# Performance work log

Hardware: AMD Instinct MI355X
Metric: run time of the kernel (lower is better)

## Reference

```python
import jax, jax.numpy as jnp
import numpy as np

EPS = 1e-8
B, S1, S2, D, H, L, NCLS = 4, 256, 256, 300, 256, 10, 22
AGG_IN = 2 + 3 * 2 * L  # cos max/mean + (maxpool, attentive, max-attentive) x (fw,bw) x l = 62


def _lstm_dir(x, Wih, Whh, b):
    # x: (batch, seq, in); PyTorch gate order i, f, g, o
    pre = jnp.einsum('bsd,gd->bsg', x, Wih) + b
    h0 = jnp.zeros((x.shape[0], Whh.shape[1]), x.dtype)
    def step(carry, p):
        h, c = carry
        g = p + h @ Whh.T
        i, f, gg, o = jnp.split(g, 4, axis=-1)
        c = jax.nn.sigmoid(f) * c + jax.nn.sigmoid(i) * jnp.tanh(gg)
        h = jax.nn.sigmoid(o) * jnp.tanh(c)
        return (h, c), h
    (hT, _), hs = jax.lax.scan(step, (h0, h0), jnp.swapaxes(pre, 0, 1))
    return jnp.swapaxes(hs, 0, 1), hT


def bilstm(x, Wf, Uf, bf, Wb, Ub, bb):
    hs_f, hT_f = _lstm_dir(x, Wf, Uf, bf)
    hs_b, hT_b = _lstm_dir(x[:, ::-1], Wb, Ub, bb)
    return jnp.concatenate([hs_f, hs_b[:, ::-1]], -1), hT_f, hT_b


def div_small(n, d):
    return n / jnp.where(d > EPS, d, EPS)


def cos_matrix(v1, v2):
    # (b,p,h),(b,q,h) -> (b,p,q) cosine similarity matrix (attention())
    a = jnp.einsum('bph,bqh->bpq', v1, v2)
    d = jnp.linalg.norm(v1, axis=-1)[:, :, None] * jnp.linalg.norm(v2, axis=-1)[:, None, :]
    return div_small(a, d)


def mp_match(v1, v2, w):
    # mp_matching_func: cosine over h of (w*v1, w*v2) per perspective -> (b,s,l)
    w2 = w * w
    num = jnp.einsum('lh,bsh,bsh->bsl', w2, v1, v2)
    n1 = jnp.sqrt(jnp.einsum('lh,bsh->bsl', w2, v1 * v1))
    n2 = jnp.sqrt(jnp.einsum('lh,bsh->bsl', w2, v2 * v2))
    return num / jnp.maximum(n1 * n2, EPS)


def mp_match_pairwise(v1, v2, w):
    # mp_matching_func_pairwise -> (b,p,q,l)
    v1w = v1[:, None] * w[None, :, None]  # (b,l,p,h)
    v2w = v2[:, None] * w[None, :, None]  # (b,l,q,h)
    n = jnp.einsum('blph,blqh->blpq', v1w, v2w)
    d = jnp.linalg.norm(v1w, axis=-1)[:, :, :, None] * jnp.linalg.norm(v2w, axis=-1)[:, :, None, :]
    return jnp.transpose(div_small(n, d), (0, 2, 3, 1))


def bimpm_forward(left, right,
                  ctx_Wih_f, ctx_Whh_f, ctx_b_f, ctx_Wih_b, ctx_Whh_b, ctx_b_b,
                  agg_Wih_f, agg_Whh_f, agg_b_f, agg_Wih_b, agg_Whh_b, agg_b_b,
                  mp_w3, mp_w4, mp_w5, mp_w6, mp_w7, mp_w8,
                  fc1_W, fc1_b, fc2_W, fc2_b):
    cp, _, _ = bilstm(left, ctx_Wih_f, ctx_Whh_f, ctx_b_f, ctx_Wih_b, ctx_Whh_b, ctx_b_b)
    ch, _, _ = bilstm(right, ctx_Wih_f, ctx_Whh_f, ctx_b_f, ctx_Wih_b, ctx_Whh_b, ctx_b_b)
    p_fw, p_bw = jnp.split(cp, 2, -1)  # (b,p,H) each
    h_fw, h_bw = jnp.split(ch, 2, -1)  # (b,q,H) each
    att_fw = cos_matrix(p_fw, h_fw)  # also the cosine_sim used for max/mean match
    att_bw = cos_matrix(p_bw, h_bw)
    mv1 = [att_fw.max(2, keepdims=True), att_fw.mean(2, keepdims=True)]
    mv2 = [att_fw.max(1)[..., None], att_fw.mean(1)[..., None]]
    # maxpool match
    mm_fw = mp_match_pairwise(p_fw, h_fw, mp_w3)
    mm_bw = mp_match_pairwise(p_bw, h_bw, mp_w4)
    mv1 += [mm_fw.max(2), mm_bw.max(2)]
    mv2 += [mm_fw.max(1), mm_bw.max(1)]
    # attentive + max-attentive match
    def att_stats(att, vp, vh):
        mean_h = div_small(jnp.einsum('bpq,bqh->bph', att, vh), att.sum(2, keepdims=True))
        mean_p = div_small(jnp.einsum('bpq,bph->bqh', att, vp), att.sum(1)[..., None])
        max_h = jnp.max(att[..., None] * vh[:, None, :, :], axis=2)  # (b,p,H)
        max_p = jnp.max(att[..., None] * vp[:, :, None, :], axis=1)  # (b,q,H)
        return mean_h, mean_p, max_h, max_p
    mh_fw, mpv_fw, xh_fw, xp_fw = att_stats(att_fw, p_fw, h_fw)
    mh_bw, mpv_bw, xh_bw, xp_bw = att_stats(att_bw, p_bw, h_bw)
    mv1 += [mp_match(p_fw, mh_fw, mp_w5), mp_match(p_bw, mh_bw, mp_w6),
            mp_match(p_fw, xh_fw, mp_w7), mp_match(p_bw, xh_bw, mp_w8)]
    mv2 += [mp_match(h_fw, mpv_fw, mp_w5), mp_match(h_bw, mpv_bw, mp_w6),
            mp_match(h_fw, xp_fw, mp_w7), mp_match(h_bw, xp_bw, mp_w8)]
    mv_p = jnp.concatenate(mv1, -1)  # (b,p,62)
    mv_h = jnp.concatenate(mv2, -1)  # (b,q,62)
    _, ap_f, ap_b = bilstm(mv_p, agg_Wih_f, agg_Whh_f, agg_b_f, agg_Wih_b, agg_Whh_b, agg_b_b)
    _, ah_f, ah_b = bilstm(mv_h, agg_Wih_f, agg_Whh_f, agg_b_f, agg_Wih_b, agg_Whh_b, agg_b_b)
    l1, l2 = left.shape[1], right.shape[1]
    lengths = jnp.broadcast_to(jnp.array([l1 / (l1 + l2), l2 / (l1 + l2)], left.dtype), (left.shape[0], 2))
    x = jnp.concatenate([ap_f, ap_b, ah_f, ah_b, lengths, left.mean(1), right.mean(1)], -1)
    x = jnp.tanh(x @ fc1_W.T + fc1_b)
    return x @ fc2_W.T + fc2_b


def setup_inputs():
    ks = jax.random.split(jax.random.key(0), 20)
    f = lambda i, shape, s=0.1: jax.random.normal(ks[i], shape, jnp.float32) * s
    return {
        'left': jax.random.normal(ks[0], (B, S1, D), jnp.float32),
        'right': jax.random.normal(ks[1], (B, S2, D), jnp.float32),
        'ctx_Wih_f': f(2, (4 * H, D)), 'ctx_Whh_f': f(3, (4 * H, H)), 'ctx_b_f': jnp.zeros((4 * H,), jnp.float32),
        'ctx_Wih_b': f(4, (4 * H, D)), 'ctx_Whh_b': f(5, (4 * H, H)), 'ctx_b_b': jnp.zeros((4 * H,), jnp.float32),
        'agg_Wih_f': f(6, (4 * H, AGG_IN)), 'agg_Whh_f': f(7, (4 * H, H)), 'agg_b_f': jnp.zeros((4 * H,), jnp.float32),
        'agg_Wih_b': f(8, (4 * H, AGG_IN)), 'agg_Whh_b': f(9, (4 * H, H)), 'agg_b_b': jnp.zeros((4 * H,), jnp.float32),
        'mp_w3': f(10, (L, H), 0.3), 'mp_w4': f(11, (L, H), 0.3), 'mp_w5': f(12, (L, H), 0.3),
        'mp_w6': f(13, (L, H), 0.3), 'mp_w7': f(14, (L, H), 0.3), 'mp_w8': f(15, (L, H), 0.3),
        'fc1_W': f(16, (2 * H, 4 * H + 2 + 2 * D), 0.01), 'fc1_b': jnp.zeros((2 * H,), jnp.float32),
        'fc2_W': f(17, (NCLS, 2 * H), 0.01), 'fc2_b': jnp.zeros((NCLS,), jnp.float32),
    }


def reference(left, right, ctx_Wih_f, ctx_Whh_f, ctx_b_f, ctx_Wih_b, ctx_Whh_b, ctx_b_b,
              agg_Wih_f, agg_Whh_f, agg_b_f, agg_Wih_b, agg_Whh_b, agg_b_b,
              mp_w3, mp_w4, mp_w5, mp_w6, mp_w7, mp_w8, fc1_W, fc1_b, fc2_W, fc2_b):
    return bimpm_forward(left, right, ctx_Wih_f, ctx_Whh_f, ctx_b_f, ctx_Wih_b, ctx_Whh_b, ctx_b_b,
                         agg_Wih_f, agg_Whh_f, agg_b_f, agg_Wih_b, agg_Whh_b, agg_b_b,
                         mp_w3, mp_w4, mp_w5, mp_w6, mp_w7, mp_w8, fc1_W, fc1_b, fc2_W, fc2_b)
```

## Files before the change

kernel.cpp:

```cpp
#include <hip/hip_runtime.h>
#include <hip/hip_bf16.h>
#include <math.h>

#define EPSV 1e-8f

__device__ __forceinline__ float dsmall(float d){ return d > EPSV ? d : EPSV; }
__device__ __forceinline__ float sigf(float x){ return 1.f/(1.f+expf(-x)); }

__global__ __launch_bounds__(1024) void k_transpose2(const float* __restrict__ WF,
                                                     const float* __restrict__ WB,
                                                     float* __restrict__ WT0,
                                                     float* __restrict__ WT1){
  const float* W = blockIdx.z ? WB : WF;
  float* WT = blockIdx.z ? WT1 : WT0;
  __shared__ float t[32][33];
  int rb = blockIdx.y*32, cb = blockIdx.x*32;
  int r = rb + threadIdx.y, c = cb + threadIdx.x;
  t[threadIdx.y][threadIdx.x] = W[(size_t)r*256 + c];
  __syncthreads();
  int rr = cb + threadIdx.y, cc = rb + threadIdx.x;
  WT[(size_t)rr*1024 + cc] = t[threadIdx.x][threadIdx.y];
}

__global__ __launch_bounds__(256) void k_proj(
    const float* __restrict__ left, const float* __restrict__ right,
    const float* __restrict__ WihF, const float* __restrict__ WihB,
    const float* __restrict__ bF, const float* __restrict__ bB,
    float* __restrict__ PREf, float* __restrict__ PREb)
{
  const int z = blockIdx.z, zo = z >> 1, zi = z & 1;
  const float* A = zo ? right : left;
  const float* B = zi ? WihB : WihF;
  const float* bias = zi ? bB : bF;
  float* C = (zi ? PREb : PREf) + (size_t)zo*1048576;
  const int K = 300;

  __shared__ float As[16][68];
  __shared__ float Bs[16][68];
  const int mb = blockIdx.y*64, nb = blockIdx.x*64;
  const int tid = threadIdx.x;
  const int tx = tid & 15, ty = tid >> 4;

  float acc[4][4];
  #pragma unroll
  for (int i=0;i<4;i++)
    #pragma unroll
    for (int j=0;j<4;j++) acc[i][j] = 0.f;

  for (int kt = 0; kt < K; kt += 16) {
    int ka = tid & 15, ma = tid >> 4;
    #pragma unroll
    for (int q=0;q<4;q++){
      int m = ma + q*16;
      float v = 0.f, bvv = 0.f;
      if (kt+ka < K){
        v = A[(size_t)(mb+m)*300 + kt+ka];
        bvv = B[(size_t)(nb+m)*300 + kt+ka];
      }
      As[ka][m] = v; Bs[ka][m] = bvv;
    }
    __syncthreads();
    #pragma unroll
    for (int k=0;k<16;k++){
      float a[4], bv[4];
      #pragma unroll
      for (int i=0;i<4;i++) a[i] = As[k][ty*4+i];
      #pragma unroll
      for (int j=0;j<4;j++) bv[j] = Bs[k][tx*4+j];
      #pragma unroll
      for (int i=0;i<4;i++)
        #pragma unroll
        for (int j=0;j<4;j++) acc[i][j] += a[i]*bv[j];
    }
    __syncthreads();
  }
  #pragma unroll
  for (int i=0;i<4;i++){
    int m = mb + ty*4 + i;
    #pragma unroll
    for (int j=0;j<4;j++){
      int n = nb + tx*4 + j;
      C[(size_t)m*1024 + n] = acc[i][j] + bias[n];
    }
  }
}

__global__ __launch_bounds__(256) void k_aggproj(
    const float* __restrict__ MV_,
    const float* __restrict__ WihF, const float* __restrict__ WihB,
    const float* __restrict__ bF, const float* __restrict__ bB,
    float* __restrict__ PREf, float* __restrict__ PREb)
{
  const int zi = blockIdx.z;
  const float* B = zi ? WihB : WihF;
  const float* bias = zi ? bB : bF;
  float* C = zi ? PREb : PREf;
  const int K = 62;

  __shared__ float As[16][68];
  __shared__ float Bs[16][68];
  const int mb = blockIdx.y*64, nb = blockIdx.x*64;
  const int tid = threadIdx.x;
  const int tx = tid & 15, ty = tid >> 4;

  float acc[4][4];
  #pragma unroll
  for (int i=0;i<4;i++)
    #pragma unroll
    for (int j=0;j<4;j++) acc[i][j] = 0.f;

  for (int kt = 0; kt < K; kt += 16) {
    int ka = tid & 15, ma = tid >> 4;
    #pragma unroll
    for (int q=0;q<4;q++){
      int m = ma + q*16;
      float v = 0.f, bvv = 0.f;
      if (kt+ka < K){
        v = MV_[(size_t)(mb+m)*62 + kt+ka];
        bvv = B[(size_t)(nb+m)*62 + kt+ka];
      }
      As[ka][m] = v; Bs[ka][m] = bvv;
    }
    __syncthreads();
    #pragma unroll
    for (int k=0;k<16;k++){
      float a[4], bv[4];
      #pragma unroll
      for (int i=0;i<4;i++) a[i] = As[k][ty*4+i];
      #pragma unroll
      for (int j=0;j<4;j++) bv[j] = Bs[k][tx*4+j];
      #pragma unroll
      for (int i=0;i<4;i++)
        #pragma unroll
        for (int j=0;j<4;j++) acc[i][j] += a[i]*bv[j];
    }
    __syncthreads();
  }
  #pragma unroll
  for (int i=0;i<4;i++){
    int m = mb + ty*4 + i;
    #pragma unroll
    for (int j=0;j<4;j++){
      int n = nb + tx*4 + j;
      C[(size_t)m*1024 + n] = acc[i][j] + bias[n];
    }
  }
}

__global__ __launch_bounds__(256) void k_att(
    const float* __restrict__ HS_, const float* __restrict__ NORM_,
    float* __restrict__ ATT_)
{
  const int z = blockIdx.z;
  const int d = z >> 2, b = z & 3;
  const float* A = HS_ + d*256 + (size_t)b*131072;
  const float* B = HS_ + 524288 + d*256 + (size_t)b*131072;
  const float* Uv = NORM_ + (size_t)b*512 + d*256;
  const float* Vv = NORM_ + (size_t)(4+b)*512 + d*256;
  float* C = ATT_ + (size_t)z*65536;

  __shared__ float As[16][68];
  __shared__ float Bs[16][68];
  const int mb = blockIdx.y*64, nb = blockIdx.x*64;
  const int tid = threadIdx.x;
  const int tx = tid & 15, ty = tid >> 4;

  float acc[4][4];
  #pragma unroll
  for (int i=0;i<4;i++)
    #pragma unroll
    for (int j=0;j<4;j++) acc[i][j] = 0.f;

  for (int kt = 0; kt < 256; kt += 16) {
    int ka = tid & 15, ma = tid >> 4;
    #pragma unroll
    for (int q=0;q<4;q++){
      int m = ma + q*16;
      As[ka][m] = A[(size_t)(mb+m)*512 + kt+ka];
      Bs[ka][m] = B[(size_t)(nb+m)*512 + kt+ka];
    }
    __syncthreads();
    #pragma unroll
    for (int k=0;k<16;k++){
      float a[4], bv[4];
      #pragma unroll
      for (int i=0;i<4;i++) a[i] = As[k][ty*4+i];
      #pragma unroll
      for (int j=0;j<4;j++) bv[j] = Bs[k][tx*4+j];
      #pragma unroll
      for (int i=0;i<4;i++)
        #pragma unroll
        for (int j=0;j<4;j++) acc[i][j] += a[i]*bv[j];
    }
    __syncthreads();
  }
  #pragma unroll
  for (int i=0;i<4;i++){
    int m = mb + ty*4 + i;
    float um = Uv[m];
    #pragma unroll
    for (int j=0;j<4;j++){
      int n = nb + tx*4 + j;
      C[(size_t)m*256 + n] = acc[i][j] / dsmall(um * Vv[n]);
    }
  }
}

__global__ __launch_bounds__(256) void k_attstat(
    const float* __restrict__ ATT_, const float* __restrict__ HS_,
    const float* __restrict__ RS_, const float* __restrict__ CS_,
    float* __restrict__ MEANH_, float* __restrict__ XH_,
    float* __restrict__ MEANP_, float* __restrict__ XP_)
{
  const int z16 = blockIdx.z;
  const int var = z16 >> 3;
  const int z = z16 & 7;
  const int d = z >> 2, b = z & 3;
  const float* A = ATT_ + (size_t)z*65536;
  const float* B = (var ? HS_ : HS_ + 524288) + d*256 + (size_t)b*131072;
  const float* U = (var ? CS_ : RS_) + z*256;
  float* C1 = (var ? MEANP_ : MEANH_) + (size_t)z*65536;
  float* C2 = (var ? XP_    : XH_   ) + (size_t)z*65536;

  __shared__ float As[16][68];
  __shared__ float Bs[16][68];
  const int mb = blockIdx.y*64, nb = blockIdx.x*64;
  const int tid = threadIdx.x;
  const int tx = tid & 15, ty = tid >> 4;

  float asum[4][4], amax[4][4];
  #pragma unroll
  for (int i=0;i<4;i++)
    #pragma unroll
    for (int j=0;j<4;j++){ asum[i][j]=0.f; amax[i][j]=-INFINITY; }

  for (int kt = 0; kt < 256; kt += 16) {
    if (var == 0) {
      int ka = tid & 15, ma = tid >> 4;
      #pragma unroll
      for (int q=0;q<4;q++)
        As[ka][ma+q*16] = A[(size_t)(mb+ma+q*16)*256 + kt+ka];
    } else {
      int ma = tid & 63, ka = tid >> 6;
      #pragma unroll
      for (int q=0;q<4;q++)
        As[ka+q*4][ma] = A[(size_t)(kt+ka+q*4)*256 + mb+ma];
    }
    {
      int nbi = tid & 63, kb = tid >> 6;
      #pragma unroll
      for (int q=0;q<4;q++)
        Bs[kb+q*4][nbi] = B[(size_t)(kt+kb+q*4)*512 + nb+nbi];
    }
    __syncthreads();
    #pragma unroll
    for (int k=0;k<16;k++){
      float a[4], bv[4];
      #pragma unroll
      for (int i=0;i<4;i++) a[i] = As[k][ty*4+i];
      #pragma unroll
      for (int j=0;j<4;j++) bv[j] = Bs[k][tx*4+j];
      #pragma unroll
      for (int i=0;i<4;i++)
        #pragma unroll
        for (int j=0;j<4;j++){
          float p = a[i]*bv[j];
          asum[i][j] += p;
          amax[i][j] = fmaxf(amax[i][j], p);
        }
    }
    __syncthreads();
  }
  #pragma unroll
  for (int i=0;i<4;i++){
    int m = mb + ty*4 + i;
    float ud = dsmall(U[m]);
    #pragma unroll
    for (int j=0;j<4;j++){
      int n = nb + tx*4 + j;
      C1[(size_t)m*256 + n] = asum[i][j] / ud;
      C2[(size_t)m*256 + n] = amax[i][j];
    }
  }
}

__global__ __launch_bounds__(256) void k_pmm2(
    const float* __restrict__ HS_,
    const float* __restrict__ w3, const float* __restrict__ w4,
    const float* __restrict__ WN1_, const float* __restrict__ WN2_,
    float* __restrict__ PARTR, float* __restrict__ PARTC)
{
  const int z = blockIdx.z;
  const int dir = z >= 40;
  const int zz = z - dir*40;
  const int bq = zz / 10, l = zz % 10;
  const float* A = HS_ + dir*256 + (size_t)bq*131072;
  const float* B = HS_ + 524288 + dir*256 + (size_t)bq*131072;
  const float* Wv = (dir ? w4 : w3) + l*256;
  const float* U = WN1_ + dir*10240 + bq*2560 + l*256;
  const float* V = WN2_ + dir*10240 + bq*2560 + l*256;

  __shared__ float As[16][68];
  __shared__ float Bs[16][68];
  const int mb = blockIdx.y*64, nb = blockIdx.x*64;
  const int tid = threadIdx.x;
  const int tx = tid & 15, ty = tid >> 4;

  float acc[4][4];
  #pragma unroll
  for (int i=0;i<4;i++)
    #pragma unroll
    for (int j=0;j<4;j++) acc[i][j] = 0.f;

  for (int kt = 0; kt < 256; kt += 16) {
    int ka = tid & 15, ma = tid >> 4;
    float w = Wv[kt+ka]; float w2 = w*w;
    #pragma unroll
    for (int q=0;q<4;q++){
      As[ka][ma+q*16] = A[(size_t)(mb+ma+q*16)*512 + kt+ka] * w2;
      Bs[ka][ma+q*16] = B[(size_t)(nb+ma+q*16)*512 + kt+ka];
    }
    __syncthreads();
    #pragma unroll
    for (int k=0;k<16;k++){
      float a[4], bv[4];
      #pragma unroll
      for (int i=0;i<4;i++) a[i] = As[k][ty*4+i];
      #pragma unroll
      for (int j=0;j<4;j++) bv[j] = Bs[k][tx*4+j];
      #pragma unroll
      for (int i=0;i<4;i++)
        #pragma unroll
        for (int j=0;j<4;j++) acc[i][j] += a[i]*bv[j];
    }
    __syncthreads();
  }
  float um[4], vn[4];
  #pragma unroll
  for (int i=0;i<4;i++) um[i] = U[mb + ty*4 + i];
  #pragma unroll
  for (int j=0;j<4;j++) vn[j] = V[nb + tx*4 + j];
  float c[4][4];
  #pragma unroll
  for (int i=0;i<4;i++)
    #pragma unroll
    for (int j=0;j<4;j++) c[i][j] = acc[i][j] / dsmall(um[i]*vn[j]);

  float rm[4];
  #pragma unroll
  for (int i=0;i<4;i++){
    rm[i] = fmaxf(fmaxf(c[i][0], c[i][1]), fmaxf(c[i][2], c[i][3]));
    rm[i] = fmaxf(rm[i], __shfl_xor(rm[i], 1, 64));
    rm[i] = fmaxf(rm[i], __shfl_xor(rm[i], 2, 64));
    rm[i] = fmaxf(rm[i], __shfl_xor(rm[i], 4, 64));
    rm[i] = fmaxf(rm[i], __shfl_xor(rm[i], 8, 64));
  }
  if ((tid & 15) == 0){
    #pragma unroll
    for (int i=0;i<4;i++)
      PARTR[((size_t)z*4 + blockIdx.x)*256 + mb + ty*4 + i] = rm[i];
  }
  __syncthreads();
  float* colp = &As[0][0];
  #pragma unroll
  for (int j=0;j<4;j++)
    colp[ty*64 + tx*4 + j] = fmaxf(fmaxf(c[0][j], c[1][j]), fmaxf(c[2][j], c[3][j]));
  __syncthreads();
  if (tid < 64){
    float m = colp[tid];
    #pragma unroll
    for (int r=1;r<16;r++) m = fmaxf(m, colp[r*64 + tid]);
    PARTC[((size_t)z*4 + blockIdx.y)*256 + nb + tid] = m;
  }
}

__global__ void k_pcomb(const float* __restrict__ PARTR, const float* __restrict__ PARTC,
                        float* __restrict__ MMRo, float* __restrict__ MMCo){
  int z = blockIdx.x, i = threadIdx.x;
  size_t b0 = (size_t)z*4*256 + i;
  float r = fmaxf(fmaxf(PARTR[b0], PARTR[b0+256]), fmaxf(PARTR[b0+512], PARTR[b0+768]));
  float c = fmaxf(fmaxf(PARTC[b0], PARTC[b0+256]), fmaxf(PARTC[b0+512], PARTC[b0+768]));
  MMRo[(size_t)z*256 + i] = r;
  MMCo[(size_t)z*256 + i] = c;
}

__global__ __launch_bounds__(256, 1) void k_scanaux(
    const float* __restrict__ PREf, const float* __restrict__ PREb,
    const float* __restrict__ WTf, const float* __restrict__ WTb,
    float* __restrict__ Hbuf, int* __restrict__ flg,
    float* __restrict__ HSo, float* __restrict__ HTo,
    int do_aux,
    const float* __restrict__ fc1W, float* __restrict__ W1T,
    const float* __restrict__ aWhhF, float* __restrict__ WTaggF,
    const float* __restrict__ aWhhB, float* __restrict__ WTaggB,
    const float* __restrict__ left, const float* __restrict__ right,
    float* __restrict__ XM)
{
  __shared__ float Wl[256][128];
  __shared__ float hl[256];
  __shared__ float red[4][4][40];

  const int bx = blockIdx.x;
  const int tid = threadIdx.x;

  if (bx >= 128) {
    if (!do_aux) return;
    float (*tl)[33] = (float(*)[33])Wl;
    const int aux = bx - 128;
    for (int u = aux; u < 816 + 512 + 8; u += 64) {
      if (u < 816) {
        int tI = u % 16, tJ = u / 16;
        int r0 = tI*32, c0 = tJ*32;
        for (int e = tid; e < 1024; e += 256) {
          int rr = e >> 5, cc = e & 31;
          int c = c0 + cc;
          tl[rr][cc] = (c < 1626) ? fc1W[(size_t)(r0+rr)*1626 + c] : 0.f;
        }
        __syncthreads();
        for (int e = tid; e < 1024; e += 256) {
          int cc = e >> 5, rr = e & 31;
          int c = c0 + cc;
          if (c < 1626) W1T[(size_t)c*512 + r0 + rr] = tl[rr][cc];
        }
        __syncthreads();
      } else if (u < 1328) {
        int u2 = u - 816;
        const float* S = (u2 >= 256) ? aWhhB : aWhhF;
        float* D = (u2 >= 256) ? WTaggB : WTaggF;
        int tile = u2 & 255;
        int r0 = (tile >> 3)*32, c0 = (tile & 7)*32;
        for (int e = tid; e < 1024; e += 256) {
          int rr = e >> 5, cc = e & 31;
          tl[rr][cc] = S[(size_t)(r0+rr)*256 + c0 + cc];
        }
        __syncthreads();
        for (int e = tid; e < 1024; e += 256) {
          int cc = e >> 5, rr = e & 31;
          D[(size_t)(c0+cc)*1024 + r0 + rr] = tl[rr][cc];
        }
        __syncthreads();
      } else {
        int m = u - 1328;
        int b = m & 3, sideR = m >> 2;
        const float* src = sideR ? right : left;
        for (int ch = tid; ch < 300; ch += 256) {
          float s = 0.f;
          for (int t = 0; t < 256; t++) s += src[((size_t)(b*256+t))*300 + ch];
          XM[b*600 + sideR*300 + ch] = s * (1.f/256.f);
        }
      }
    }
    return;
  }

  const int team = bx & 15;
  const int d  = team >> 3;
  const int sq = team & 7;
  const int wg = bx >> 4;
  const float* PRE = d ? PREb : PREf;
  const float* WT  = d ? WTb  : WTf;
  float* Hb = Hbuf + (size_t)team*512;
  int* fl = flg + team*256;

  const int kc = tid >> 5;
  const int gq = tid & 31;
  const int aj = tid & 31;

  for (int e = tid; e < 256*128; e += 256) {
    int k = e >> 7, c = e & 127;
    Wl[k][c] = WT[(size_t)k*1024 + (c>>5)*256 + wg*32 + (c&31)];
  }
  if (tid < 256) hl[tid] = 0.f;
  float cst = 0.f;
  __syncthreads();

  for (int tt = 0; tt < 256; ++tt) {
    const int t = d ? 255 - tt : tt;
    const int wp = tt & 1;
    const int sp = (tt + 1) & 1;

    float pre0=0.f, pre1=0.f, pre2=0.f, pre3=0.f;
    if (tid < 32) {
      const size_t pbase = ((size_t)(sq*256 + t))*1024 + wg*32 + aj;
      pre0 = PRE[pbase];       pre1 = PRE[pbase + 256];
      pre2 = PRE[pbase + 512]; pre3 = PRE[pbase + 768];
    }

    if (tt > 0 && kc != wg) {
      const int* flp = &fl[kc*32];
      while (__hip_atomic_load(flp, __ATOMIC_RELAXED, __HIP_MEMORY_SCOPE_AGENT) < tt)
        __builtin_amdgcn_s_sleep(1);
      float v = __hip_atomic_load(&Hb[sp*256 + kc*32 + gq],
                                  __ATOMIC_RELAXED, __HIP_MEMORY_SCOPE_AGENT);
      hl[kc*32 + gq] = v;
    }

    float acc[4] = {0.f, 0.f, 0.f, 0.f};
    #pragma unroll 8
    for (int kk = 0; kk < 32; ++kk) {
      const int k = kc*32 + kk;
      float4 w = *(const float4*)&Wl[k][gq*4];
      float h = hl[k];
      acc[0] += h*w.x; acc[1] += h*w.y; acc[2] += h*w.z; acc[3] += h*w.w;
    }
    #pragma unroll
    for (int c2=0;c2<4;c2++)
      acc[c2] += __shfl_xor(acc[c2], 32, 64);
    if ((tid & 32) == 0) {
      const int kp = kc >> 1;
      #pragma unroll
      for (int c2=0;c2<4;c2++)
        red[kp][c2][gq] = acc[c2];
    }
    __syncthreads();

    float hreg = 0.f;
    if (tid < 32) {
      float g[4];
      #pragma unroll
      for (int gt=0; gt<4; ++gt) {
        const int c = gt*32 + aj;
        const int gqq = c >> 2, cc = c & 3;
        g[gt] = red[0][cc][gqq] + red[1][cc][gqq] + red[2][cc][gqq] + red[3][cc][gqq];
      }
      g[0] += pre0; g[1] += pre1; g[2] += pre2; g[3] += pre3;
      const float ig = sigf(g[0]), fg = sigf(g[1]), gg = tanhf(g[2]), og = sigf(g[3]);
      cst = fg*cst + ig*gg;
      hreg = og*tanhf(cst);
      hl[wg*32 + aj] = hreg;
      __hip_atomic_store(&Hb[wp*256 + wg*32 + aj], hreg,
                         __ATOMIC_RELAXED, __HIP_MEMORY_SCOPE_AGENT);
    }
    __syncthreads();

    if (tid == 0)
      __hip_atomic_store(&fl[wg*32], tt+1, __ATOMIC_RELAXED, __HIP_MEMORY_SCOPE_AGENT);

    if (tid < 32) {
      if (HSo) HSo[((size_t)(sq*256 + t))*512 + d*256 + wg*32 + aj] = hreg;
      if (HTo && tt == 255) HTo[((size_t)(sq*2 + d))*256 + wg*32 + aj] = hreg;
    }
  }
}

__global__ __launch_bounds__(256) void k_norms(const float* __restrict__ HS_,
                                               const float* __restrict__ w3, const float* __restrict__ w4,
                                               float* __restrict__ NORM_,
                                               float* __restrict__ WN1_, float* __restrict__ WN2_){
  const int bx = blockIdx.x;
  int lane = threadIdx.x & 63;
  if (bx < 1024) {
    int r = bx*4 + (threadIdx.x >> 6);
    int seq = r >> 9, d = (r >> 8) & 1, i = r & 255;
    const float* row = HS_ + ((size_t)(seq*256 + i))*512 + d*256;
    float s = 0.f;
    #pragma unroll
    for (int q=0;q<4;q++){ float v = row[lane + 64*q]; s += v*v; }
    for (int off=32; off; off>>=1) s += __shfl_xor(s, off, 64);
    if (lane == 0) NORM_[r] = sqrtf(s);
  } else {
    int rid = (bx-1024)*4 + (threadIdx.x >> 6);
    int side = rid / 20480; int rem = rid % 20480;
    int d = rem / 10240; int rem2 = rem % 10240;
    int b = rem2 / 2560; int l = (rem2 / 256) % 10; int i = rem2 & 255;
    int seq = side ? 4+b : b;
    const float* row = HS_ + ((size_t)(seq*256 + i))*512 + d*256;
    const float* w = (d ? w4 : w3) + l*256;
    float s = 0.f;
    #pragma unroll
    for (int q=0;q<4;q++){ float wv = w[lane+64*q]; float v = row[lane+64*q]; s += wv*wv*v*v; }
    for (int off=32; off; off>>=1) s += __shfl_xor(s, off, 64);
    if (lane == 0) (side ? WN2_ : WN1_)[rem] = sqrtf(s);
  }
}

__global__ __launch_bounds__(256) void k_redcomb(const float* __restrict__ ATT_,
                                                 float* __restrict__ RS_, float* __restrict__ RMAX_,
                                                 float* __restrict__ CS_, float* __restrict__ CMAX_){
  const int bx = blockIdx.x;
  if (bx < 512) {
    int r = bx*4 + (threadIdx.x >> 6);
    int lane = threadIdx.x & 63;
    const float* row = ATT_ + (size_t)r*256;
    float s = 0.f, m = -INFINITY;
    #pragma unroll
    for (int q=0;q<4;q++){ float v = row[lane + 64*q]; s += v; m = fmaxf(m,v); }
    for (int off=32; off; off>>=1){ s += __shfl_xor(s,off,64); m = fmaxf(m, __shfl_xor(m,off,64)); }
    if (lane == 0){ RS_[r] = s; RMAX_[r] = m; }
  } else {
    int z = bx - 512;
    const float* in = ATT_ + (size_t)z*65536;
    int j = threadIdx.x;
    float s = 0.f, m = -INFINITY;
    for (int r=0;r<256;r++){ float v = in[(size_t)r*256 + j]; s += v; m = fmaxf(m,v); }
    CS_[z*256 + j] = s;
    CMAX_[z*256 + j] = m;
  }
}

__global__ __launch_bounds__(256) void k_mv(
    const float* __restrict__ HS_, const float* __restrict__ MEANH_, const float* __restrict__ MEANP_,
    const float* __restrict__ XH_, const float* __restrict__ XP_,
    const float* __restrict__ RS_, const float* __restrict__ RMAX_,
    const float* __restrict__ CS_, const float* __restrict__ CMAX_,
    const float* __restrict__ MMR_, const float* __restrict__ MMC_,
    const float* __restrict__ w5, const float* __restrict__ w6,
    const float* __restrict__ w7, const float* __restrict__ w8,
    float* __restrict__ MV_)
{
  const int blk = blockIdx.x;
  const int side = blk >> 10, b = (blk >> 8) & 3, i = blk & 255;
  const int wv = threadIdx.x >> 6, lane = threadIdx.x & 63;
  float* mvrow = MV_ + (size_t)blk*62;

  if (threadIdx.x == 0){
    const float* rmax = side ? CMAX_ : RMAX_;
    const float* rsum = side ? CS_   : RS_;
    mvrow[0] = rmax[b*256 + i];
    mvrow[1] = rsum[b*256 + i] * (1.f/256.f);
  }
  if (threadIdx.x < 20){
    int dd = threadIdx.x / 10, l = threadIdx.x % 10;
    const float* mm = side ? MMC_ : MMR_;
    mvrow[2 + dd*10 + l] = mm[dd*10240 + (b*10 + l)*256 + i];
  }
  const int d = wv & 1;
  const int seq = side ? 4+b : b;
  const float* arow = HS_ + ((size_t)(seq*256 + i))*512 + d*256;
  const float* Mside = side ? MEANP_ : MEANH_;
  const float* Xside = side ? XP_ : XH_;
  const float* brow = (wv < 2 ? Mside : Xside) + (size_t)d*262144 + (size_t)b*65536 + (size_t)i*256;
  const float* wp = (wv==0) ? w5 : (wv==1) ? w6 : (wv==2) ? w7 : w8;

  float av[4], bv[4];
  #pragma unroll
  for (int q=0;q<4;q++){ av[q] = arow[lane+64*q]; bv[q] = brow[lane+64*q]; }
  for (int l=0;l<10;l++){
    const float* wrow = wp + l*256;
    float s1=0.f, s2=0.f, s3=0.f;
    #pragma unroll
    for (int q=0;q<4;q++){
      float w = wrow[lane+64*q]; float w2v = w*w;
      s1 += w2v*av[q]*bv[q]; s2 += w2v*av[q]*av[q]; s3 += w2v*bv[q]*bv[q];
    }
    for (int off=32; off; off>>=1){
      s1 += __shfl_xor(s1,off,64); s2 += __shfl_xor(s2,off,64); s3 += __shfl_xor(s3,off,64);
    }
    if (lane == 0) mvrow[22 + wv*10 + l] = s1 / fmaxf(sqrtf(s2)*sqrtf(s3), EPSV);
  }
}

__global__ __launch_bounds__(512) void k_fc12(const float* __restrict__ HT_,
                                              const float* __restrict__ XM,
                                              const float* __restrict__ W1T,
                                              const float* __restrict__ b1,
                                              const float* __restrict__ W2,
                                              const float* __restrict__ b2,
                                              float* __restrict__ out){
  __shared__ float x[1626];
  __shared__ float xs2[512];
  int b = blockIdx.x, t = threadIdx.x;
  if (t < 256){
    x[t]       = HT_[(b*2+0)*256 + t];
    x[256+t]   = HT_[(b*2+1)*256 + t];
    x[512+t]   = HT_[((4+b)*2+0)*256 + t];
    x[768+t]   = HT_[((4+b)*2+1)*256 + t];
  }
  if (t == 0){ x[1024] = 0.5f; x[1025] = 0.5f; }
  if (t < 300){ x[1026+t] = XM[b*600 + t]; x[1326+t] = XM[b*600 + 300 + t]; }
  __syncthreads();
  float acc = b1[t];
  for (int k=0;k<1626;k++) acc += x[k]*W1T[(size_t)k*512 + t];
  xs2[t] = tanhf(acc);
  __syncthreads();
  if (t < 22){
    float o = b2[t];
    const float* wr = W2 + (size_t)t*512;
    for (int k=0;k<512;k++) o += xs2[k]*wr[k];
    out[b*22 + t] = o;
  }
}

extern "C" void kernel_launch(void* const* d_in, const int* in_sizes, int n_in,
                              void* d_out, int out_size, void* d_ws, size_t ws_size,
                              hipStream_t stream) {
  const float* left  = (const float*)d_in[0];
  const float* right = (const float*)d_in[1];
  const float* cWihF = (const float*)d_in[2];
  const float* cWhhF = (const float*)d_in[3];
  const float* cbF   = (const float*)d_in[4];
  const float* cWihB = (const float*)d_in[5];
  const float* cWhhB = (const float*)d_in[6];
  const float* cbB   = (const float*)d_in[7];
  const float* aWihF = (const float*)d_in[8];
  const float* aWhhF = (const float*)d_in[9];
  const float* abF   = (const float*)d_in[10];
  const float* aWihB = (const float*)d_in[11];
  const float* aWhhB = (const float*)d_in[12];
  const float* abB   = (const float*)d_in[13];
  const float* w3 = (const float*)d_in[14];
  const float* w4 = (const float*)d_in[15];
  const float* w5 = (const float*)d_in[16];
  const float* w6 = (const float*)d_in[17];
  const float* w7 = (const float*)d_in[18];
  const float* w8 = (const float*)d_in[19];
  const float* fc1W = (const float*)d_in[20];
  const float* fc1b = (const float*)d_in[21];
  const float* fc2W = (const float*)d_in[22];
  const float* fc2b = (const float*)d_in[23];
  float* out = (float*)d_out;
  float* ws = (float*)d_ws;

  float* WT    = ws;
  float* PREf  = ws + 1048576;
  float* PREb  = ws + 3145728;
  float* HS    = ws + 5242880;
  float* NORM  = ws + 6291456;
  float* ATT   = ws + 6295552;
  float* RS    = ws + 6819840;
  float* RMAX  = ws + 6821888;
  float* CS    = ws + 6823936;
  float* CMAX  = ws + 6825984;
  float* MEANH = ws + 6828032;
  float* MEANP = ws + 7352320;
  float* XH    = ws + 7876608;
  float* XP    = ws + 8400896;
  float* WN1   = ws + 8925184;
  float* WN2   = ws + 8945664;
  float* MM    = ws + 8966144;
  float* MMR   = ws + 11587584;
  float* MMC   = ws + 11608064;
  float* MV    = ws + 11628544;
  float* HT    = ws + 11755520;
  float* XM    = ws + 11759616;
  float* W1T   = ws + 11764064;

  float* HXB  = MM;
  int*   FLG  = (int*)(MM + 8192);
  float* PARTR= MM;
  float* PARTC= MM + 81920;

  k_transpose2<<<dim3(8,32,2), dim3(32,32), 0, stream>>>(cWhhF, cWhhB, WT, WT + 262144);

  k_proj<<<dim3(16,16,4),256,0,stream>>>(left, right, cWihF, cWihB, cbF, cbB, PREf, PREb);

  hipMemsetAsync(FLG, 0, 4096*sizeof(int), stream);
  k_scanaux<<<192,256,0,stream>>>(PREf, PREb, WT, WT+262144, HXB, FLG, HS, nullptr,
                                  1, fc1W, W1T, aWhhF, WT+524288, aWhhB, WT+786432,
                                  left, right, XM);

  k_norms<<<11264,256,0,stream>>>(HS, w3, w4, NORM, WN1, WN2);

  k_att<<<dim3(4,4,8),256,0,stream>>>(HS, NORM, ATT);

  k_redcomb<<<520,256,0,stream>>>(ATT, RS, RMAX, CS, CMAX);

  k_attstat<<<dim3(4,4,16),256,0,stream>>>(ATT, HS, RS, CS, MEANH, XH, MEANP, XP);

  k_pmm2<<<dim3(4,4,80),256,0,stream>>>(HS, w3, w4, WN1, WN2, PARTR, PARTC);
  k_pcomb<<<80,256,0,stream>>>(PARTR, PARTC, MMR, MMC);

  k_mv<<<2048,256,0,stream>>>(HS, MEANH, MEANP, XH, XP, RS, RMAX, CS, CMAX,
                              MMR, MMC, w5, w6, w7, w8, MV);

  k_aggproj<<<dim3(16,32,2),256,0,stream>>>(MV, aWihF, aWihB, abF, abB, PREf, PREb);

  hipMemsetAsync(FLG, 0, 4096*sizeof(int), stream);
  k_scanaux<<<192,256,0,stream>>>(PREf, PREb, WT+524288, WT+786432, HXB, FLG, nullptr, HT,
                                  0, fc1W, W1T, aWhhF, WT+524288, aWhhB, WT+786432,
                                  left, right, XM);

  k_fc12<<<4,512,0,stream>>>(HT, XM, W1T, fc1b, fc2W, fc2b, out);
}
```

Baseline: 1.357 ms.

## Fuse attention row/col reductions into k_att epilogue and relax scan step barrier

Measured after the change: 1.497 ms. 10.4% more time.

```diff
diff --git a/kernel.cpp b/kernel.cpp
--- a/kernel.cpp
+++ b/kernel.cpp
@@ -149,7 +149,9 @@
 
 __global__ __launch_bounds__(256) void k_att(
     const float* __restrict__ HS_, const float* __restrict__ NORM_,
-    float* __restrict__ ATT_)
+    float* __restrict__ ATT_,
+    float* __restrict__ PRS, float* __restrict__ PRM,
+    float* __restrict__ PCS, float* __restrict__ PCM)
 {
   const int z = blockIdx.z;
   const int d = z >> 2, b = z & 3;
@@ -194,6 +196,7 @@
     }
     __syncthreads();
   }
+  float c[4][4];
   #pragma unroll
   for (int i=0;i<4;i++){
     int m = mb + ty*4 + i;
@@ -201,9 +204,59 @@
     #pragma unroll
     for (int j=0;j<4;j++){
       int n = nb + tx*4 + j;
-      C[(size_t)m*256 + n] = acc[i][j] / dsmall(um * Vv[n]);
-    }
-  }
+      c[i][j] = acc[i][j] / dsmall(um * Vv[n]);
+      C[(size_t)m*256 + n] = c[i][j];
+    }
+  }
+  float rs[4], rm[4];
+  #pragma unroll
+  for (int i=0;i<4;i++){
+    rs[i] = c[i][0]+c[i][1]+c[i][2]+c[i][3];
+    rm[i] = fmaxf(fmaxf(c[i][0], c[i][1]), fmaxf(c[i][2], c[i][3]));
+    rs[i] += __shfl_xor(rs[i], 1, 64); rm[i] = fmaxf(rm[i], __shfl_xor(rm[i], 1, 64));
+    rs[i] += __shfl_xor(rs[i], 2, 64); rm[i] = fmaxf(rm[i], __shfl_xor(rm[i], 2, 64));
+    rs[i] += __shfl_xor(rs[i], 4, 64); rm[i] = fmaxf(rm[i], __shfl_xor(rm[i], 4, 64));
+    rs[i] += __shfl_xor(rs[i], 8, 64); rm[i] = fmaxf(rm[i], __shfl_xor(rm[i], 8, 64));
+  }
+  if ((tid & 15) == 0){
+    #pragma unroll
+    for (int i=0;i<4;i++){
+      PRS[((size_t)z*4 + blockIdx.x)*256 + mb + ty*4 + i] = rs[i];
+      PRM[((size_t)z*4 + blockIdx.x)*256 + mb + ty*4 + i] = rm[i];
+    }
+  }
+  __syncthreads();
+  float* csum = &As[0][0];
+  float* cmax = &Bs[0][0];
+  #pragma unroll
+  for (int j=0;j<4;j++){
+    csum[ty*64 + tx*4 + j] = c[0][j]+c[1][j]+c[2][j]+c[3][j];
+    cmax[ty*64 + tx*4 + j] = fmaxf(fmaxf(c[0][j], c[1][j]), fmaxf(c[2][j], c[3][j]));
+  }
+  __syncthreads();
+  if (tid < 64){
+    float s = 0.f, m = -INFINITY;
+    #pragma unroll
+    for (int r=0;r<16;r++){ s += csum[r*64 + tid]; m = fmaxf(m, cmax[r*64 + tid]); }
+    PCS[((size_t)z*4 + blockIdx.y)*256 + nb + tid] = s;
+    PCM[((size_t)z*4 + blockIdx.y)*256 + nb + tid] = m;
+  }
+}
+
+__global__ void k_attcomb(const float* __restrict__ PRS, const float* __restrict__ PRM,
+                          const float* __restrict__ PCS, const float* __restrict__ PCM,
+                          float* __restrict__ RS_, float* __restrict__ RMAX_,
+                          float* __restrict__ CS_, float* __restrict__ CMAX_){
+  int z = blockIdx.x, j = threadIdx.x;
+  float rs=0.f, rm=-INFINITY, cs=0.f, cm=-INFINITY;
+  #pragma unroll
+  for (int p=0;p<4;p++){
+    size_t o = ((size_t)z*4 + p)*256 + j;
+    rs += PRS[o]; rm = fmaxf(rm, PRM[o]);
+    cs += PCS[o]; cm = fmaxf(cm, PCM[o]);
+  }
+  RS_[z*256 + j] = rs;  RMAX_[z*256 + j] = rm;
+  CS_[z*256 + j] = cs;  CMAX_[z*256 + j] = cm;
 }
 
 __global__ __launch_bounds__(256) void k_attstat(
@@ -470,7 +523,7 @@
     int k = e >> 7, c = e & 127;
     Wl[k][c] = WT[(size_t)k*1024 + (c>>5)*256 + wg*32 + (c&31)];
   }
-  if (tid < 256) hl[tid] = 0.f;
+  hl[tid] = 0.f;
   float cst = 0.f;
   __syncthreads();
 
@@ -531,15 +584,16 @@
       __hip_atomic_store(&Hb[wp*256 + wg*32 + aj], hreg,
                          __ATOMIC_RELAXED, __HIP_MEMORY_SCOPE_AGENT);
     }
-    __syncthreads();
-
-    if (tid == 0)
-      __hip_atomic_store(&fl[wg*32], tt+1, __ATOMIC_RELAXED, __HIP_MEMORY_SCOPE_AGENT);
-
+    if (tid < 64) {
+      asm volatile("s_waitcnt vmcnt(0)" ::: "memory");
+      if (tid == 0)
+        __hip_atomic_store(&fl[wg*32], tt+1, __ATOMIC_RELAXED, __HIP_MEMORY_SCOPE_AGENT);
+    }
     if (tid < 32) {
       if (HSo) HSo[((size_t)(sq*256 + t))*512 + d*256 + wg*32 + aj] = hreg;
       if (HTo && tt == 255) HTo[((size_t)(sq*2 + d))*256 + wg*32 + aj] = hreg;
     }
+    __syncthreads();
   }
 }
 
@@ -571,30 +625,6 @@
     for (int q=0;q<4;q++){ float wv = w[lane+64*q]; float v = row[lane+64*q]; s += wv*wv*v*v; }
     for (int off=32; off; off>>=1) s += __shfl_xor(s, off, 64);
     if (lane == 0) (side ? WN2_ : WN1_)[rem] = sqrtf(s);
-  }
-}
-
-__global__ __launch_bounds__(256) void k_redcomb(const float* __restrict__ ATT_,
-                                                 float* __restrict__ RS_, float* __restrict__ RMAX_,
-                                                 float* __restrict__ CS_, float* __restrict__ CMAX_){
-  const int bx = blockIdx.x;
-  if (bx < 512) {
-    int r = bx*4 + (threadIdx.x >> 6);
-    int lane = threadIdx.x & 63;
-    const float* row = ATT_ + (size_t)r*256;
-    float s = 0.f, m = -INFINITY;
-    #pragma unroll
-    for (int q=0;q<4;q++){ float v = row[lane + 64*q]; s += v; m = fmaxf(m,v); }
-    for (int off=32; off; off>>=1){ s += __shfl_xor(s,off,64); m = fmaxf(m, __shfl_xor(m,off,64)); }
-    if (lane == 0){ RS_[r] = s; RMAX_[r] = m; }
-  } else {
-    int z = bx - 512;
-    const float* in = ATT_ + (size_t)z*65536;
-    int j = threadIdx.x;
-    float s = 0.f, m = -INFINITY;
-    for (int r=0;r<256;r++){ float v = in[(size_t)r*256 + j]; s += v; m = fmaxf(m,v); }
-    CS_[z*256 + j] = s;
-    CMAX_[z*256 + j] = m;
   }
 }
 
@@ -737,6 +767,10 @@
 
   float* HXB  = MM;
   int*   FLG  = (int*)(MM + 8192);
+  float* PRS  = MM;
+  float* PRM  = MM + 8192;
+  float* PCS  = MM + 16384;
+  float* PCM  = MM + 24576;
   float* PARTR= MM;
   float* PARTC= MM + 81920;
 
@@ -751,9 +785,8 @@
 
   k_norms<<<11264,256,0,stream>>>(HS, w3, w4, NORM, WN1, WN2);
 
-  k_att<<<dim3(4,4,8),256,0,stream>>>(HS, NORM, ATT);
-
-  k_redcomb<<<520,256,0,stream>>>(ATT, RS, RMAX, CS, CMAX);
+  k_att<<<dim3(4,4,8),256,0,stream>>>(HS, NORM, ATT, PRS, PRM, PCS, PCM);
+  k_attcomb<<<8,256,0,stream>>>(PRS, PRM, PCS, PCM, RS, RMAX, CS, CMAX);
 
   k_attstat<<<dim3(4,4,16),256,0,stream>>>(ATT, HS, RS, CS, MEANH, XH, MEANP, XP);
 
```
